# Optimization experiments

Hardware: AMD Instinct MI355X
Metric: run time of the kernel (lower is better)

The kernel has to match this reference:

```python
import jax, jax.numpy as jnp
import numpy as np

B, K, DIM = 65536, 512, 128
EPS = 1e-8
LN_2PI = 1.83787706641


def setup_inputs() -> dict:
    key = jax.random.key(0)
    k1, k2, k3 = jax.random.split(key, 3)
    x = jax.random.normal(k1, (B, DIM), dtype=jnp.float32)
    centers = jax.random.uniform(k2, (K, DIM), dtype=jnp.float32)
    # torch init: 0.2 * rand + 0.9
    D_param = 0.2 * jax.random.uniform(k3, (K, DIM), dtype=jnp.float32) + 0.9
    return {"x": x, "centers": centers, "D_param": D_param}


def reference(x, centers, D_param):
    Bc, dim = x.shape
    Kc = centers.shape[0]
    Dabs = jnp.abs(D_param) + EPS          # [K, D]
    Dinv = 1.0 / Dabs                       # diagonal Sigma^{-1}
    log_det = jnp.sum(jnp.log(Dabs), axis=1)  # [K]
    dsf = -0.5 * log_det
    det_scale_safe = jnp.exp(dsf - jnp.max(dsf))  # [K]

    # dist_sq[b,k] = sum_d (x[b,d]-c[k,d])^2 * Dinv[k,d], via GEMM expansion
    # (avoids the [B,K,D] diff tensor the torch loop materializes)
    dist_sq = ((x * x) @ Dinv.T
               - 2.0 * (x @ (centers * Dinv).T)
               + jnp.sum(centers * centers * Dinv, axis=1)[None, :])  # [B, K]

    expo_gmm = -0.5 * dist_sq
    expo_cmm = jnp.power(dist_sq + 1.0, -((1.0 + dim) / 2.0))

    def log_resp(expo):
        safe = expo - jnp.max(expo, axis=-1, keepdims=True)
        numer = det_scale_safe[None, :] * jnp.exp(safe)
        denom = jnp.sum(numer, axis=1, keepdims=True)
        return jnp.log(jnp.clip(numer / denom, 1e-8))

    resp_gmm = log_resp(expo_gmm)
    resp_cmm = log_resp(expo_cmm)

    assign = jnp.argmax(resp_gmm, axis=1)                    # [B]
    onehot = jax.nn.one_hot(assign, Kc, dtype=expo_gmm.dtype)  # [B, K]
    ce = -0.5 * dim * LN_2PI + log_det[None, :] + expo_gmm
    # torch multiplies onehot twice; onehot^2 == onehot
    ce = (-1.0 / Bc) * jnp.sum(onehot * ce)

    # return_gmm and return_cmm both True
    a = jax.nn.softmax(resp_gmm, axis=-1)
    b = jax.nn.softmax(resp_cmm, axis=-1)
    resp = jnp.log((a + b) / 2.0)
    return resp, ce
```

## Files before the change

kernel.cpp:

```cpp
#include <hip/hip_runtime.h>
#include <math.h>

#define NROWS 65536
#define KCL   512
#define NDIM  128
#define CE_IDX ((size_t)NROWS * (size_t)KCL)
#define LN_2PI 1.83787706641f

using f32x4  = __attribute__((ext_vector_type(4))) float;
using short8 = __attribute__((ext_vector_type(8))) short;

__device__ __forceinline__ unsigned short f2bf(float f) {
    unsigned u = __float_as_uint(f);
    return (unsigned short)((u + 0x7fffu + ((u >> 16) & 1u)) >> 16);
}

__device__ __forceinline__ unsigned cvt_pk_bf16(float lo, float hi) {
    unsigned r;
    asm("v_cvt_pk_bf16_f32 %0, %1, %2" : "=v"(r) : "v"(lo), "v"(hi));
    return r;
}

__device__ __forceinline__ void gld_lds16(const void* g, void* l) {
    __builtin_amdgcn_global_load_lds(
        (const __attribute__((address_space(1))) unsigned int*)g,
        (__attribute__((address_space(3))) unsigned int*)l,
        16, 0, 0);
}

__global__ void k_prep(const float* __restrict__ centers,
                       const float* __restrict__ Dp,
                       unsigned short* __restrict__ W,
                       float* __restrict__ log_det,
                       float* __restrict__ cdotc,
                       float* __restrict__ ce_slot) {
    int n = blockIdx.x;
    int d = threadIdx.x;
    int t = n >> 4, m = n & 15;
    float Dabs = fabsf(Dp[n * NDIM + d]) + 1e-8f;
    float dinv = 1.0f / Dabs;
    float c = centers[n * NDIM + d];
    int j1 = d, j2 = 128 + d;
    W[t * 4096 + (j1 >> 3) * 128 + m * 8 + (j1 & 7)] = f2bf(-2.0f * c * dinv);
    W[t * 4096 + (j2 >> 3) * 128 + m * 8 + (j2 & 7)] = f2bf(dinv);
    float lg = logf(Dabs);
    float cc = c * c * dinv;
    #pragma unroll
    for (int s = 32; s >= 1; s >>= 1) {
        lg += __shfl_xor(lg, s);
        cc += __shfl_xor(cc, s);
    }
    __shared__ float sred[4];
    if ((d & 63) == 0) { sred[(d >> 6) * 2 + 0] = lg; sred[(d >> 6) * 2 + 1] = cc; }
    __syncthreads();
    if (d == 0) {
        log_det[n] = sred[0] + sred[2];
        cdotc[n]   = sred[1] + sred[3];
        if (n == 0) *ce_slot = 0.0f;
    }
}

__global__ __launch_bounds__(512) __attribute__((amdgpu_waves_per_eu(4, 8)))
void k_main(const float* __restrict__ x,
            const unsigned short* __restrict__ W,
            const float* __restrict__ log_det,
            const float* __restrict__ cdotc,
            float* __restrict__ out) {
    __shared__ __align__(16) short ldsW[3][8192];
    __shared__ float s_cd[KCL], s_ld[KCL], s_ds[KCL];
    __shared__ float ex_mn[2][64], ex_key[2][64], ex_ds[2][64], ex_sg[2][64];
    __shared__ float sred[8], ce_part[4];
    __shared__ float s_invsum;

    const int tid = threadIdx.x;
    {
        float ldv = log_det[tid];
        float cdv = cdotc[tid];
        s_ld[tid] = ldv;
        s_cd[tid] = cdv;
        float e = __expf(-0.5f * ldv);
        s_ds[tid] = e;
        float s = e;
        #pragma unroll
        for (int sh = 32; sh >= 1; sh >>= 1) s += __shfl_xor(s, sh);
        if ((tid & 63) == 0) sred[tid >> 6] = s;
    }

    const int lane = tid & 63;
    const int w = __builtin_amdgcn_readfirstlane(tid >> 6);
    const int g = w >> 1;
    const int h = w & 1;
    const int m = lane & 15;
    const int q = lane >> 4;
    const int r0 = blockIdx.x * 64;

    const float* xp = x + (size_t)(r0 + g * 16 + m) * NDIM + q * 8;
    short8 afx[4], afxx[4];
    #pragma unroll
    for (int kk = 0; kk < 4; kk++) {
        float4 a0 = *(const float4*)(xp + kk * 32);
        float4 a1 = *(const float4*)(xp + kk * 32 + 4);
        union { unsigned u[4]; short8 s; } A, AX;
        A.u[0]  = cvt_pk_bf16(a0.x, a0.y);
        A.u[1]  = cvt_pk_bf16(a0.z, a0.w);
        A.u[2]  = cvt_pk_bf16(a1.x, a1.y);
        A.u[3]  = cvt_pk_bf16(a1.z, a1.w);
        AX.u[0] = cvt_pk_bf16(a0.x * a0.x, a0.y * a0.y);
        AX.u[1] = cvt_pk_bf16(a0.z * a0.z, a0.w * a0.w);
        AX.u[2] = cvt_pk_bf16(a1.x * a1.x, a1.y * a1.y);
        AX.u[3] = cvt_pk_bf16(a1.z * a1.z, a1.w * a1.w);
        afx[kk] = A.s; afxx[kk] = AX.s;
    }

    f32x4 acc[16];
    #pragma unroll
    for (int t = 0; t < 16; t++) acc[t] = (f32x4){0.f, 0.f, 0.f, 0.f};

    const char* gWb = (const char*)W + ((w & 4) ? 16 * 8192 : 0)
                      + (w & 3) * 2048 + (size_t)lane * 16;
    char* lW0 = (char*)&ldsW[0][0] + w * 2048;

    gld_lds16(gWb, lW0);
    gld_lds16(gWb + 1024, lW0 + 1024);
    gld_lds16(gWb + 8192, lW0 + 16384);
    gld_lds16(gWb + 8192 + 1024, lW0 + 16384 + 1024);
    asm volatile("s_waitcnt vmcnt(2) lgkmcnt(0)" ::: "memory");
    __builtin_amdgcn_s_barrier();
    asm volatile("" ::: "memory");

    if (tid == 0) {
        float tot = 0.0f;
        #pragma unroll
        for (int i = 0; i < 8; i++) tot += sred[i];
        s_invsum = 1.0f / tot;
    }

    #pragma unroll
    for (int u = 0; u < 16; ++u) {
        if (u < 14) {
            const char* s = gWb + (size_t)(u + 2) * 8192;
            char* l = (char*)&ldsW[0][0] + ((u + 2) % 3) * 16384 + w * 2048;
            gld_lds16(s, l);
            gld_lds16(s + 1024, l + 1024);
        }
        const short* lb = &ldsW[u % 3][h * 4096];
        __builtin_amdgcn_s_setprio(1);
        #pragma unroll
        for (int kk = 0; kk < 4; kk++) {
            short8 b0 = *(const short8*)(lb + kk * 512 + lane * 8);
            short8 b1 = *(const short8*)(lb + 2048 + kk * 512 + lane * 8);
            acc[u] = __builtin_amdgcn_mfma_f32_16x16x32_bf16(afx[kk],  b0, acc[u], 0, 0, 0);
            acc[u] = __builtin_amdgcn_mfma_f32_16x16x32_bf16(afxx[kk], b1, acc[u], 0, 0, 0);
        }
        __builtin_amdgcn_s_setprio(0);
        if (u < 14) {
            asm volatile("s_waitcnt vmcnt(2)" ::: "memory");
        } else if (u == 14) {
            asm volatile("s_waitcnt vmcnt(0)" ::: "memory");
        }
        if (u < 15) {
            __builtin_amdgcn_s_barrier();
            asm volatile("" ::: "memory");
        }
    }

    const int colbase = h * 256 + m;
    float mn[4], bkey[4], bds[4];
    #pragma unroll
    for (int r = 0; r < 4; r++) { mn[r] = INFINITY; bkey[r] = INFINITY; bds[r] = 0.f; }
    #pragma unroll
    for (int u = 0; u < 16; u++) {
        const int col = colbase + u * 16;
        float cd = s_cd[col], ldc = s_ld[col];
        #pragma unroll
        for (int r = 0; r < 4; r++) {
            float ds = acc[u][r] + cd;
            acc[u][r] = ds;
            mn[r] = fminf(mn[r], ds);
            float key = ds + ldc;
            bool t = key < bkey[r];
            bkey[r] = t ? key : bkey[r];
            bds[r]  = t ? ds  : bds[r];
        }
    }
    #pragma unroll
    for (int s = 1; s < 16; s <<= 1) {
        #pragma unroll
        for (int r = 0; r < 4; r++) {
            mn[r] = fminf(mn[r], __shfl_xor(mn[r], s));
            float ok = __shfl_xor(bkey[r], s);
            float od = __shfl_xor(bds[r],  s);
            bool t = ok < bkey[r];
            bkey[r] = t ? ok : bkey[r];
            bds[r]  = t ? od : bds[r];
        }
    }
    const int rowb = g * 16 + q * 4;
    if (m == 0) {
        #pragma unroll
        for (int r = 0; r < 4; r++) {
            ex_mn[h][rowb + r]  = mn[r];
            ex_key[h][rowb + r] = bkey[r];
            ex_ds[h][rowb + r]  = bds[r];
        }
    }
    __syncthreads();

    float hmn[4], pay[4], Sg[4];
    #pragma unroll
    for (int r = 0; r < 4; r++) {
        mn[r] = fminf(mn[r], ex_mn[h ^ 1][rowb + r]);
        float ok = ex_key[h ^ 1][rowb + r];
        float od = ex_ds[h ^ 1][rowb + r];
        bool t = h ? (ok <= bkey[r]) : (ok < bkey[r]);
        float bk = t ? ok : bkey[r];
        float bd = t ? od : bds[r];
        pay[r] = fmaf(-1.5f, bd, bk);
        hmn[r] = 0.5f * mn[r];
        Sg[r] = 0.f;
    }

    #pragma unroll
    for (int u = 0; u < 16; u++) {
        float dsc = s_ds[colbase + u * 16];
        #pragma unroll
        for (int r = 0; r < 4; r++) {
            float ng = dsc * __expf(fmaf(-0.5f, acc[u][r], hmn[r]));
            Sg[r] += ng;
            acc[u][r] = ng;
        }
    }
    #pragma unroll
    for (int s = 1; s < 16; s <<= 1)
        #pragma unroll
        for (int r = 0; r < 4; r++) Sg[r] += __shfl_xor(Sg[r], s);

    if (m == 0) {
        #pragma unroll
        for (int r = 0; r < 4; r++) ex_sg[h][rowb + r] = Sg[r];
    }
    if (h == 0) {
        float ce = (pay[0] + pay[1]) + (pay[2] + pay[3]);
        if (m != 0) ce = 0.0f;
        ce += __shfl_xor(ce, 16);
        ce += __shfl_xor(ce, 32);
        if (lane == 0) ce_part[g] = ce;
    }
    __syncthreads();

    if (tid == 0) {
        float ce = (ce_part[0] + ce_part[1]) + (ce_part[2] + ce_part[3]);
        float v = (-1.0f / (float)NROWS) *
                  (ce + 64.0f * (-0.5f * (float)NDIM * LN_2PI));
        atomicAdd(out + CE_IDX, v);
    }

    float iSg05[4];
    #pragma unroll
    for (int r = 0; r < 4; r++)
        iSg05[r] = 0.5f / (Sg[r] + ex_sg[h ^ 1][rowb + r]);

    const float isum05 = 0.5f * s_invsum;
    #pragma unroll
    for (int u = 0; u < 16; u++) {
        float bt = s_ds[colbase + u * 16] * isum05;
        #pragma unroll
        for (int r = 0; r < 4; r++) {
            float z = fmaxf(acc[u][r] * iSg05[r], 5e-9f) + bt;
            out[(size_t)(r0 + g * 16 + q * 4 + r) * KCL + colbase + u * 16] = __logf(z);
        }
    }
}

extern "C" void kernel_launch(void* const* d_in, const int* in_sizes, int n_in,
                              void* d_out, int out_size, void* d_ws, size_t ws_size,
                              hipStream_t stream) {
    const float* x       = (const float*)d_in[0];
    const float* centers = (const float*)d_in[1];
    const float* Dp      = (const float*)d_in[2];
    float* out = (float*)d_out;

    unsigned short* W = (unsigned short*)d_ws;
    float* log_det = (float*)((char*)d_ws + (size_t)KCL * 256 * sizeof(unsigned short));
    float* cdotc   = log_det + KCL;

    k_prep<<<KCL, NDIM, 0, stream>>>(centers, Dp, W, log_det, cdotc, out + CE_IDX);
    k_main<<<NROWS / 64, 512, 0, stream>>>(x, W, log_det, cdotc, out);
}
```

Baseline: 196.3 us.

## Halve rows per block and split columns across four waves for occupancy

Each block now handles 32 rows instead of 64, with four waves per row group each owning a quarter of the 512 clusters. That halves the accumulator registers per wave, and the waves-per-EU hint is raised to target higher occupancy. The triple-buffered asynchronous W prefetch is replaced by a single LDS buffer that is loaded synchronously between two barriers on each step. The cross-wave reductions for min, argmax and the softmax sum now combine four partial results instead of two. This trades pipelined loads for more resident waves, and it doubles the total W traffic because there are twice as many blocks.

```diff
diff --git a/kernel.cpp b/kernel.cpp
--- a/kernel.cpp
+++ b/kernel.cpp
@@ -60,16 +60,16 @@
     }
 }
 
-__global__ __launch_bounds__(512) __attribute__((amdgpu_waves_per_eu(4, 8)))
+__global__ __launch_bounds__(512) __attribute__((amdgpu_waves_per_eu(6, 8)))
 void k_main(const float* __restrict__ x,
             const unsigned short* __restrict__ W,
             const float* __restrict__ log_det,
             const float* __restrict__ cdotc,
             float* __restrict__ out) {
-    __shared__ __align__(16) short ldsW[3][8192];
+    __shared__ __align__(16) short ldsW[16384];
     __shared__ float s_cd[KCL], s_ld[KCL], s_ds[KCL];
-    __shared__ float ex_mn[2][64], ex_key[2][64], ex_ds[2][64], ex_sg[2][64];
-    __shared__ float sred[8], ce_part[4];
+    __shared__ float ex_mn[4][32], ex_key[4][32], ex_ds[4][32], ex_sg[4][32];
+    __shared__ float sred[8], ce_part[2];
     __shared__ float s_invsum;
 
     const int tid = threadIdx.x;
@@ -88,11 +88,11 @@
 
     const int lane = tid & 63;
     const int w = __builtin_amdgcn_readfirstlane(tid >> 6);
-    const int g = w >> 1;
-    const int h = w & 1;
+    const int g  = w >> 2;
+    const int cq = w & 3;
     const int m = lane & 15;
     const int q = lane >> 4;
-    const int r0 = blockIdx.x * 64;
+    const int r0 = blockIdx.x * 32;
 
     const float* xp = x + (size_t)(r0 + g * 16 + m) * NDIM + q * 8;
     short8 afx[4], afxx[4];
@@ -112,19 +112,18 @@
         afx[kk] = A.s; afxx[kk] = AX.s;
     }
 
-    f32x4 acc[16];
-    #pragma unroll
-    for (int t = 0; t < 16; t++) acc[t] = (f32x4){0.f, 0.f, 0.f, 0.f};
-
-    const char* gWb = (const char*)W + ((w & 4) ? 16 * 8192 : 0)
-                      + (w & 3) * 2048 + (size_t)lane * 16;
-    char* lW0 = (char*)&ldsW[0][0] + w * 2048;
-
-    gld_lds16(gWb, lW0);
-    gld_lds16(gWb + 1024, lW0 + 1024);
-    gld_lds16(gWb + 8192, lW0 + 16384);
-    gld_lds16(gWb + 8192 + 1024, lW0 + 16384 + 1024);
-    asm volatile("s_waitcnt vmcnt(2) lgkmcnt(0)" ::: "memory");
+    f32x4 acc[8];
+    #pragma unroll
+    for (int v = 0; v < 8; v++) acc[v] = (f32x4){0.f, 0.f, 0.f, 0.f};
+
+    const char* gWb = (const char*)W + w * 4096 + (size_t)lane * 16;
+    char* lWb = (char*)&ldsW[0] + w * 4096;
+
+    gld_lds16(gWb,        lWb);
+    gld_lds16(gWb + 1024, lWb + 1024);
+    gld_lds16(gWb + 2048, lWb + 2048);
+    gld_lds16(gWb + 3072, lWb + 3072);
+    asm volatile("s_waitcnt vmcnt(0) lgkmcnt(0)" ::: "memory");
     __builtin_amdgcn_s_barrier();
     asm volatile("" ::: "memory");
 
@@ -136,15 +135,8 @@
     }
 
     #pragma unroll
-    for (int u = 0; u < 16; ++u) {
-        if (u < 14) {
-            const char* s = gWb + (size_t)(u + 2) * 8192;
-            char* l = (char*)&ldsW[0][0] + ((u + 2) % 3) * 16384 + w * 2048;
-            gld_lds16(s, l);
-            gld_lds16(s + 1024, l + 1024);
-        }
-        const short* lb = &ldsW[u % 3][h * 4096];
-        __builtin_amdgcn_s_setprio(1);
+    for (int u = 0; u < 8; ++u) {
+        const short* lb = &ldsW[cq * 4096];
         #pragma unroll
         for (int kk = 0; kk < 4; kk++) {
             short8 b0 = *(const short8*)(lb + kk * 512 + lane * 8);
@@ -152,30 +144,32 @@
             acc[u] = __builtin_amdgcn_mfma_f32_16x16x32_bf16(afx[kk],  b0, acc[u], 0, 0, 0);
             acc[u] = __builtin_amdgcn_mfma_f32_16x16x32_bf16(afxx[kk], b1, acc[u], 0, 0, 0);
         }
-        __builtin_amdgcn_s_setprio(0);
-        if (u < 14) {
-            asm volatile("s_waitcnt vmcnt(2)" ::: "memory");
-        } else if (u == 14) {
-            asm volatile("s_waitcnt vmcnt(0)" ::: "memory");
-        }
-        if (u < 15) {
+        if (u < 7) {
             __builtin_amdgcn_s_barrier();
             asm volatile("" ::: "memory");
-        }
-    }
-
-    const int colbase = h * 256 + m;
+            const char* s = gWb + (size_t)(u + 1) * 32768;
+            gld_lds16(s,        lWb);
+            gld_lds16(s + 1024, lWb + 1024);
+            gld_lds16(s + 2048, lWb + 2048);
+            gld_lds16(s + 3072, lWb + 3072);
+            asm volatile("s_waitcnt vmcnt(0)" ::: "memory");
+            __builtin_amdgcn_s_barrier();
+            asm volatile("" ::: "memory");
+        }
+    }
+
+    const int colbase = cq * 16 + m;
     float mn[4], bkey[4], bds[4];
     #pragma unroll
     for (int r = 0; r < 4; r++) { mn[r] = INFINITY; bkey[r] = INFINITY; bds[r] = 0.f; }
     #pragma unroll
-    for (int u = 0; u < 16; u++) {
-        const int col = colbase + u * 16;
+    for (int v = 0; v < 8; v++) {
+        const int col = colbase + v * 64;
         float cd = s_cd[col], ldc = s_ld[col];
         #pragma unroll
         for (int r = 0; r < 4; r++) {
-            float ds = acc[u][r] + cd;
-            acc[u][r] = ds;
+            float ds = acc[v][r] + cd;
+            acc[v][r] = ds;
             mn[r] = fminf(mn[r], ds);
             float key = ds + ldc;
             bool t = key < bkey[r];
@@ -199,9 +193,9 @@
     if (m == 0) {
         #pragma unroll
         for (int r = 0; r < 4; r++) {
-            ex_mn[h][rowb + r]  = mn[r];
-            ex_key[h][rowb + r] = bkey[r];
-            ex_ds[h][rowb + r]  = bds[r];
+            ex_mn[cq][rowb + r]  = mn[r];
+            ex_key[cq][rowb + r] = bkey[r];
+            ex_ds[cq][rowb + r]  = bds[r];
         }
     }
     __syncthreads();
@@ -209,25 +203,30 @@
     float hmn[4], pay[4], Sg[4];
     #pragma unroll
     for (int r = 0; r < 4; r++) {
-        mn[r] = fminf(mn[r], ex_mn[h ^ 1][rowb + r]);
-        float ok = ex_key[h ^ 1][rowb + r];
-        float od = ex_ds[h ^ 1][rowb + r];
-        bool t = h ? (ok <= bkey[r]) : (ok < bkey[r]);
-        float bk = t ? ok : bkey[r];
-        float bd = t ? od : bds[r];
+        const int row = rowb + r;
+        float g0 = fminf(ex_mn[0][row], ex_mn[1][row]);
+        float g1 = fminf(ex_mn[2][row], ex_mn[3][row]);
+        hmn[r] = 0.5f * fminf(g0, g1);
+        float bk = ex_key[0][row], bd = ex_ds[0][row];
+        #pragma unroll
+        for (int w2 = 1; w2 < 4; w2++) {
+            float ok = ex_key[w2][row], od = ex_ds[w2][row];
+            bool t = ok < bk;
+            bk = t ? ok : bk;
+            bd = t ? od : bd;
+        }
         pay[r] = fmaf(-1.5f, bd, bk);
-        hmn[r] = 0.5f * mn[r];
         Sg[r] = 0.f;
     }
 
     #pragma unroll
-    for (int u = 0; u < 16; u++) {
-        float dsc = s_ds[colbase + u * 16];
-        #pragma unroll
-        for (int r = 0; r < 4; r++) {
-            float ng = dsc * __expf(fmaf(-0.5f, acc[u][r], hmn[r]));
+    for (int v = 0; v < 8; v++) {
+        float dsc = s_ds[colbase + v * 64];
+        #pragma unroll
+        for (int r = 0; r < 4; r++) {
+            float ng = dsc * __expf(fmaf(-0.5f, acc[v][r], hmn[r]));
             Sg[r] += ng;
-            acc[u][r] = ng;
+            acc[v][r] = ng;
         }
     }
     #pragma unroll
@@ -237,9 +236,9 @@
 
     if (m == 0) {
         #pragma unroll
-        for (int r = 0; r < 4; r++) ex_sg[h][rowb + r] = Sg[r];
-    }
-    if (h == 0) {
+        for (int r = 0; r < 4; r++) ex_sg[cq][rowb + r] = Sg[r];
+    }
+    if (cq == 0) {
         float ce = (pay[0] + pay[1]) + (pay[2] + pay[3]);
         if (m != 0) ce = 0.0f;
         ce += __shfl_xor(ce, 16);
@@ -249,25 +248,28 @@
     __syncthreads();
 
     if (tid == 0) {
-        float ce = (ce_part[0] + ce_part[1]) + (ce_part[2] + ce_part[3]);
+        float ce = ce_part[0] + ce_part[1];
         float v = (-1.0f / (float)NROWS) *
-                  (ce + 64.0f * (-0.5f * (float)NDIM * LN_2PI));
+                  (ce + 32.0f * (-0.5f * (float)NDIM * LN_2PI));
         atomicAdd(out + CE_IDX, v);
     }
 
     float iSg05[4];
     #pragma unroll
-    for (int r = 0; r < 4; r++)
-        iSg05[r] = 0.5f / (Sg[r] + ex_sg[h ^ 1][rowb + r]);
+    for (int r = 0; r < 4; r++) {
+        const int row = rowb + r;
+        float st = (ex_sg[0][row] + ex_sg[1][row]) + (ex_sg[2][row] + ex_sg[3][row]);
+        iSg05[r] = 0.5f / st;
+    }
 
     const float isum05 = 0.5f * s_invsum;
     #pragma unroll
-    for (int u = 0; u < 16; u++) {
-        float bt = s_ds[colbase + u * 16] * isum05;
-        #pragma unroll
-        for (int r = 0; r < 4; r++) {
-            float z = fmaxf(acc[u][r] * iSg05[r], 5e-9f) + bt;
-            out[(size_t)(r0 + g * 16 + q * 4 + r) * KCL + colbase + u * 16] = __logf(z);
+    for (int v = 0; v < 8; v++) {
+        float bt = s_ds[colbase + v * 64] * isum05;
+        #pragma unroll
+        for (int r = 0; r < 4; r++) {
+            float z = fmaxf(acc[v][r] * iSg05[r], 5e-9f) + bt;
+            out[(size_t)(r0 + g * 16 + q * 4 + r) * KCL + colbase + v * 64] = __logf(z);
         }
     }
 }
@@ -285,5 +287,5 @@
     float* cdotc   = log_det + KCL;
 
     k_prep<<<KCL, NDIM, 0, stream>>>(centers, Dp, W, log_det, cdotc, out + CE_IDX);
-    k_main<<<NROWS / 64, 512, 0, stream>>>(x, W, log_det, cdotc, out);
-}
+    k_main<<<NROWS / 32, 512, 0, stream>>>(x, W, log_det, cdotc, out);
+}
```

Result: slower. 221.5 us (+12.8%).
